# Optimization experiments

Measured on AMD Instinct MI355X. Metric: run time of the kernel, lower is better.

Reference implementation:

```python
import jax, jax.numpy as jnp
import numpy as np

B, S, E, H = 2, 2048, 1024, 16
D = E // H  # head_dim = 64


def setup_inputs() -> dict:
    key = jax.random.key(0)
    ks = jax.random.split(key, 5)
    return {
        "hidden_states": jax.random.normal(ks[0], (B, S, E), jnp.float32),
        "c_attn_w": jax.random.normal(ks[1], (E, 3 * E), jnp.float32) * 0.02,
        "c_attn_b": jnp.zeros((3 * E,), jnp.float32),
        "c_proj_w": jax.random.normal(ks[2], (E, E), jnp.float32) * 0.02,
        "c_proj_b": jnp.zeros((E,), jnp.float32),
    }


def reference(hidden_states, c_attn_w, c_attn_b, c_proj_w, c_proj_b):
    # Conv1D: x @ w + b -> qkv [B, S, 3E]
    qkv = hidden_states @ c_attn_w + c_attn_b
    q, k, v = jnp.split(qkv, 3, axis=-1)
    # [B, H, S, D]
    q = q.reshape(B, S, H, D).transpose(0, 2, 1, 3)
    k = k.reshape(B, S, H, D).transpose(0, 2, 1, 3)
    v = v.reshape(B, S, H, D).transpose(0, 2, 1, 3)
    # scores [B, H, S, S], scaled by sqrt(head_dim)
    scores = jnp.einsum("bhqd,bhkd->bhqk", q, k) / jnp.sqrt(jnp.asarray(D, q.dtype))
    causal = jnp.tril(jnp.ones((S, S), bool))  # [S, S]
    mask_value = jnp.finfo(scores.dtype).min
    scores = jnp.where(causal, scores, mask_value)
    attn = jax.nn.softmax(scores, axis=-1)
    # attn @ V -> [B, H, S, D] -> [B, S, E]
    out = jnp.einsum("bhqk,bhkd->bhqd", attn, v)
    out = out.transpose(0, 2, 1, 3).reshape(B, S, E)
    return out @ c_proj_w + c_proj_b
```

## Files before the change

### kernel.cpp

```cpp
#include <hip/hip_runtime.h>

using bf16 = __bf16;
typedef __bf16 bf16x8 __attribute__((ext_vector_type(8)));
typedef __bf16 bf16x4 __attribute__((ext_vector_type(4)));
typedef float  f32x4  __attribute__((ext_vector_type(4)));

#define MFMA16(a, b, c) __builtin_amdgcn_mfma_f32_16x16x32_bf16((a), (b), (c), 0, 0, 0)

static constexpr int S = 2048, E = 1024;
static constexpr float CSCALE = 0.18033688011112042f;

__device__ __forceinline__ void gld16(const bf16* g, bf16* l) {
    __builtin_amdgcn_global_load_lds((const __attribute__((address_space(1))) unsigned*)g,
                                     (__attribute__((address_space(3))) unsigned*)l, 16, 0, 0);
}

__global__ __launch_bounds__(256) void k_prep(const float* __restrict__ hs, const float* __restrict__ w0,
                                              const float* __restrict__ w1, bf16* __restrict__ A0,
                                              bf16* __restrict__ Wt0, bf16* __restrict__ Wt1) {
    __shared__ float tile[64][33];
    const int bx = blockIdx.x;
    if (bx < 4096) {
        int i = (bx * 256 + threadIdx.x) * 4;
        float4 v = *(const float4*)(hs + i);
        bf16x4 o = { (bf16)v.x, (bf16)v.y, (bf16)v.z, (bf16)v.w };
        *(bf16x4*)(A0 + i) = o;
        return;
    }
    const float* in;
    bf16* outp;
    int K, N, nb, kb;
    const int j = bx - 4096;
    if (j < 1536) { in = w0; outp = Wt0; K = 1024; N = 3072; nb = j % 96; kb = j / 96; }
    else          { in = w1; outp = Wt1; K = 1024; N = 1024; nb = (j - 1536) % 32; kb = (j - 1536) / 32; }
    const int bxx = nb * 32, byy = kb * 64;
    {
        const int r0 = threadIdx.x >> 5, c = threadIdx.x & 31;
#pragma unroll
        for (int i = 0; i < 8; i++)
            tile[r0 + i * 8][c] = in[(long)(byy + r0 + i * 8) * N + bxx + c];
    }
    __syncthreads();
    {
        const int n0 = threadIdx.x >> 6, k = threadIdx.x & 63;
#pragma unroll
        for (int i = 0; i < 8; i++) {
            const int n = n0 + i * 4;
            outp[(long)(bxx + n) * K + byy + k] = (bf16)tile[k][n];
        }
    }
}

__global__ __launch_bounds__(256) void k_gemm_qkv(const bf16* __restrict__ A, const bf16* __restrict__ Bt,
                                                  const float* __restrict__ bias, bf16* __restrict__ Qs,
                                                  bf16* __restrict__ Kf, bf16* __restrict__ Vf, int Kk) {
    const int bm = blockIdx.x * 128;
    const int bn = blockIdx.y * 128;
    const int tid = threadIdx.x;
    const int w = tid >> 6, lane = tid & 63;
    const int wm = (w >> 1) * 64, wn = (w & 1) * 64;
    const int col = lane & 15, quad = lane >> 4;

    __shared__ __align__(16) char smem[32768];
    bf16* sA = (bf16*)smem;
    bf16* sB = (bf16*)(smem + 16384);
    bf16* T  = (bf16*)smem;

    const bf16* pA[4]; const bf16* pB[4]; bf16* lA[4]; bf16* lB[4];
#pragma unroll
    for (int i = 0; i < 4; i++) {
        const int c = i * 256 + w * 64 + lane;
        const int r = c >> 3, sl = (c & 7) ^ (r & 7);
        pA[i] = A  + (long)(bm + r) * Kk + sl * 8;
        pB[i] = Bt + (long)(bn + r) * Kk + sl * 8;
        lA[i] = sA + i * 2048 + w * 512;
        lB[i] = sB + i * 2048 + w * 512;
    }

    f32x4 acc[4][4] = {};

    for (int k0 = 0; k0 < Kk; k0 += 64) {
        __syncthreads();
#pragma unroll
        for (int i = 0; i < 4; i++) gld16(pA[i] + k0, lA[i]);
#pragma unroll
        for (int i = 0; i < 4; i++) gld16(pB[i] + k0, lB[i]);
        __syncthreads();
#pragma unroll
        for (int h = 0; h < 2; h++) {
            bf16x8 af[4], bfr[4];
#pragma unroll
            for (int mt = 0; mt < 4; mt++) {
                const int row = wm + mt * 16 + col;
                af[mt] = *(const bf16x8*)(sA + row * 64 + (((h * 4 + quad) ^ (col & 7)) * 8));
            }
#pragma unroll
            for (int nt = 0; nt < 4; nt++) {
                const int row = wn + nt * 16 + col;
                bfr[nt] = *(const bf16x8*)(sB + row * 64 + (((h * 4 + quad) ^ (col & 7)) * 8));
            }
#pragma unroll
            for (int mt = 0; mt < 4; mt++)
#pragma unroll
                for (int nt = 0; nt < 4; nt++)
                    acc[mt][nt] = MFMA16(af[mt], bfr[nt], acc[mt][nt]);
        }
    }

    const int seg = bn >> 10;
    const int b = bm >> 11;
    const int kt0 = (bm & 2047) >> 6;

    if (seg == 0) {
#pragma unroll
        for (int mt = 0; mt < 4; mt++) {
            const int gr = bm + wm + mt * 16 + quad * 4;
#pragma unroll
            for (int nt = 0; nt < 4; nt++) {
                const int gc = bn + wn + nt * 16 + col;
                const float bv = bias[gc];
#pragma unroll
                for (int r = 0; r < 4; r++)
                    Qs[(long)(gr + r) * 1024 + gc] = (bf16)((acc[mt][nt][r] + bv) * CSCALE);
            }
        }
        return;
    }

    const int hl = w >> 1;
    if (seg == 1) {
        const int bh = b * 16 + (bn >> 6) - 16 + hl;
#pragma unroll 1
        for (int p = 0; p < 2; p++) {
            __syncthreads();
            if ((wm >> 6) == p) {
#pragma unroll
                for (int mt = 0; mt < 4; mt++) {
                    const int sl = mt * 16 + quad * 4;
#pragma unroll
                    for (int nt = 0; nt < 4; nt++) {
                        const int gcl = wn + nt * 16 + col;
                        const float bv = bias[bn + gcl];
#pragma unroll
                        for (int r = 0; r < 4; r++)
                            T[(sl + r) * 136 + gcl] = (bf16)(acc[mt][nt][r] + bv);
                    }
                }
            }
            __syncthreads();
            const int ktp = kt0 + p;
#pragma unroll
            for (int mi = 0; mi < 2; mi++) {
                const int mt = (w & 1) * 2 + mi;
#pragma unroll
                for (int half = 0; half < 2; half++) {
                    bf16x8 ch = *(const bf16x8*)(T + (mt * 16 + col) * 136 + hl * 64 + half * 32 + quad * 8);
                    const long chunk = ((long)(bh * 32 + ktp) * 8 + mt * 2 + half) * 64 + lane;
                    *(bf16x8*)(Kf + chunk * 8) = ch;
                }
            }
        }
    } else {
        const int bh = b * 16 + (bn >> 6) - 32 + hl;
#pragma unroll 1
        for (int p = 0; p < 2; p++) {
            __syncthreads();
            if ((wm >> 6) == p) {
#pragma unroll
                for (int mt = 0; mt < 4; mt++) {
                    const int sl = mt * 16 + quad * 4;
#pragma unroll
                    for (int nt = 0; nt < 4; nt++) {
                        const int gcl = wn + nt * 16 + col;
                        const float bv = bias[bn + gcl];
                        bf16x4 pk = { (bf16)(acc[mt][nt][0] + bv), (bf16)(acc[mt][nt][1] + bv),
                                      (bf16)(acc[mt][nt][2] + bv), (bf16)(acc[mt][nt][3] + bv) };
                        *(bf16x4*)(T + gcl * 72 + sl) = pk;
                    }
                }
            }
            __syncthreads();
            const int ktp = kt0 + p;
#pragma unroll
            for (int di = 0; di < 2; di++) {
                const int dt = (w & 1) * 2 + di;
#pragma unroll
                for (int ks = 0; ks < 2; ks++) {
                    bf16x8 ch = *(const bf16x8*)(T + (hl * 64 + dt * 16 + col) * 72 + ks * 32 + quad * 8);
                    const long chunk = ((long)(bh * 32 + ktp) * 8 + dt * 2 + ks) * 64 + lane;
                    *(bf16x8*)(Vf + chunk * 8) = ch;
                }
            }
        }
    }
}

__global__ __launch_bounds__(256) void k_gemm_bt64(const bf16* __restrict__ A, const bf16* __restrict__ Bt,
                                                    const float* __restrict__ bias, float* __restrict__ Cout,
                                                    int Mm, int Nn, int Kk) {
    const int bm = blockIdx.x * 64;
    const int bn = blockIdx.y * 128;
    const int tid = threadIdx.x;
    const int w = tid >> 6, lane = tid & 63;
    const int wm = (w >> 1) * 32, wn = (w & 1) * 64;
    const int col = lane & 15, quad = lane >> 4;

    __shared__ bf16 sA[64 * 64];
    __shared__ bf16 sB[128 * 64];

    const bf16* pA[2]; bf16* lA[2];
#pragma unroll
    for (int i = 0; i < 2; i++) {
        const int c = i * 256 + w * 64 + lane;
        const int r = c >> 3, sl = (c & 7) ^ (r & 7);
        pA[i] = A + (long)(bm + r) * Kk + sl * 8;
        lA[i] = sA + i * 2048 + w * 512;
    }
    const bf16* pB[4]; bf16* lB[4];
#pragma unroll
    for (int i = 0; i < 4; i++) {
        const int c = i * 256 + w * 64 + lane;
        const int r = c >> 3, sl = (c & 7) ^ (r & 7);
        pB[i] = Bt + (long)(bn + r) * Kk + sl * 8;
        lB[i] = sB + i * 2048 + w * 512;
    }

    f32x4 acc[2][4] = {};

    for (int k0 = 0; k0 < Kk; k0 += 64) {
        __syncthreads();
#pragma unroll
        for (int i = 0; i < 2; i++) gld16(pA[i] + k0, lA[i]);
#pragma unroll
        for (int i = 0; i < 4; i++) gld16(pB[i] + k0, lB[i]);
        __syncthreads();
#pragma unroll
        for (int h = 0; h < 2; h++) {
            bf16x8 af[2], bfr[4];
#pragma unroll
            for (int mt = 0; mt < 2; mt++) {
                const int row = wm + mt * 16 + col;
                af[mt] = *(const bf16x8*)(sA + row * 64 + (((h * 4 + quad) ^ (col & 7)) * 8));
            }
#pragma unroll
            for (int nt = 0; nt < 4; nt++) {
                const int row = wn + nt * 16 + col;
                bfr[nt] = *(const bf16x8*)(sB + row * 64 + (((h * 4 + quad) ^ (col & 7)) * 8));
            }
#pragma unroll
            for (int mt = 0; mt < 2; mt++)
#pragma unroll
                for (int nt = 0; nt < 4; nt++)
                    acc[mt][nt] = MFMA16(af[mt], bfr[nt], acc[mt][nt]);
        }
    }

#pragma unroll
    for (int mt = 0; mt < 2; mt++) {
        const int gr = bm + wm + mt * 16 + quad * 4;
#pragma unroll
        for (int nt = 0; nt < 4; nt++) {
            const int gc = bn + wn + nt * 16 + col;
            const float bv = bias[gc];
#pragma unroll
            for (int r = 0; r < 4; r++)
                Cout[(long)(gr + r) * Nn + gc] = acc[mt][nt][r] + bv;
        }
    }
}

__global__ __launch_bounds__(128, 2) void k_attn(const bf16* __restrict__ Qs, const bf16* __restrict__ Kf,
                                                 const bf16* __restrict__ Vf, bf16* __restrict__ out) {
    const int bh = blockIdx.x & 31;
    const int t = blockIdx.x >> 5;
    const int b = bh >> 4, h = bh & 15;
    const int tid = threadIdx.x;
    const int w = tid >> 6, lane = tid & 63;
    const int col = lane & 15, quad = lane >> 4;
    const int q0 = t * 64;
    const int nkt = t + 1;
    const int kA = nkt >> 1;
    const int kbeg = w ? kA : 0;
    const int kend = w ? nkt : kA;

    __shared__ bf16 sP[2][4096];
    __shared__ float M[64][73];
    bf16* pw = sP[w];

    const bf16* kfb = Kf + ((long)bh << 17) + lane * 8;
    const bf16* vfb = Vf + ((long)bh << 17) + lane * 8;

    bf16x8 bq[4][2];
#pragma unroll
    for (int qg = 0; qg < 4; qg++) {
        const bf16* qp = Qs + (long)(b * S + q0 + qg * 16 + col) * E + h * 64 + quad * 8;
        bq[qg][0] = *(const bf16x8*)(qp);
        bq[qg][1] = *(const bf16x8*)(qp + 32);
    }
    float m_[4] = { -1e30f, -1e30f, -1e30f, -1e30f }, l_[4] = { 0.f, 0.f, 0.f, 0.f };
    f32x4 o[4][4] = {};

#pragma unroll 1
    for (int kt = kbeg; kt < kend; kt++) {
        bf16x8 kfr[4][2], vfr[4][2];
#pragma unroll
        for (int mt = 0; mt < 4; mt++)
#pragma unroll
            for (int half = 0; half < 2; half++)
                kfr[mt][half] = *(const bf16x8*)(kfb + ((long)(kt * 8 + mt * 2 + half) << 9));
#pragma unroll
        for (int dt = 0; dt < 4; dt++)
#pragma unroll
            for (int ks = 0; ks < 2; ks++)
                vfr[dt][ks] = *(const bf16x8*)(vfb + ((long)(kt * 8 + dt * 2 + ks) << 9));

#pragma unroll
        for (int qg = 0; qg < 4; qg++) {
            f32x4 s[4];
#pragma unroll
            for (int mt = 0; mt < 4; mt++) {
                f32x4 z = {};
                z = MFMA16(kfr[mt][0], bq[qg][0], z);
                z = MFMA16(kfr[mt][1], bq[qg][1], z);
                s[mt] = z;
            }
            if (kt == nkt - 1) {
                const int qrow = q0 + qg * 16 + col;
#pragma unroll
                for (int mt = 0; mt < 4; mt++)
#pragma unroll
                    for (int r = 0; r < 4; r++)
                        if (kt * 64 + mt * 16 + quad * 4 + r > qrow) s[mt][r] = -1e30f;
            }
            float cm = -1e30f;
#pragma unroll
            for (int mt = 0; mt < 4; mt++)
#pragma unroll
                for (int r = 0; r < 4; r++) cm = fmaxf(cm, s[mt][r]);
            cm = fmaxf(cm, __shfl_xor(cm, 16));
            cm = fmaxf(cm, __shfl_xor(cm, 32));
            const float mnew = fmaxf(m_[qg], cm);
            const float alpha = __builtin_amdgcn_exp2f(m_[qg] - mnew);
            m_[qg] = mnew;
            float rs = 0.f;
#pragma unroll
            for (int mt = 0; mt < 4; mt++)
#pragma unroll
                for (int r = 0; r < 4; r++) {
                    float pe = __builtin_amdgcn_exp2f(s[mt][r] - mnew);
                    s[mt][r] = pe;
                    rs += pe;
                }
            l_[qg] = l_[qg] * alpha + rs;
#pragma unroll
            for (int dt = 0; dt < 4; dt++)
#pragma unroll
                for (int r = 0; r < 4; r++) o[qg][dt][r] *= alpha;
            const int q = qg * 16 + col;
#pragma unroll
            for (int mt = 0; mt < 4; mt++) {
                const int cl = mt * 2 + (quad >> 1);
                bf16x4 pk = { (bf16)s[mt][0], (bf16)s[mt][1], (bf16)s[mt][2], (bf16)s[mt][3] };
                *(bf16x4*)(pw + q * 64 + ((cl ^ (q & 7)) * 8 + (quad & 1) * 4)) = pk;
            }
        }
#pragma unroll
        for (int ks = 0; ks < 2; ks++) {
#pragma unroll
            for (int qg = 0; qg < 4; qg++) {
                const int q = qg * 16 + col;
                const bf16x8 ap = *(const bf16x8*)(pw + q * 64 + (((ks * 4 + quad) ^ (q & 7)) * 8));
#pragma unroll
                for (int dt = 0; dt < 4; dt++)
                    o[qg][dt] = MFMA16(vfr[dt][ks], ap, o[qg][dt]);
            }
        }
    }

#pragma unroll
    for (int qg = 0; qg < 4; qg++) {
        float lt = l_[qg];
        lt += __shfl_xor(lt, 16);
        lt += __shfl_xor(lt, 32);
        l_[qg] = lt;
    }

    if (w == 0) {
#pragma unroll
        for (int qg = 0; qg < 4; qg++) {
#pragma unroll
            for (int dt = 0; dt < 4; dt++)
#pragma unroll
                for (int r = 0; r < 4; r++)
                    M[lane][(qg * 4 + dt) * 4 + r] = o[qg][dt][r];
            M[lane][64 + qg * 2] = m_[qg];
            M[lane][65 + qg * 2] = l_[qg];
        }
    }
    __syncthreads();
    if (w == 1) {
#pragma unroll
        for (int qg = 0; qg < 4; qg++) {
            const float m0 = M[lane][64 + qg * 2];
            const float l0 = M[lane][65 + qg * 2];
            const float mm = fmaxf(m0, m_[qg]);
            const float a0 = __builtin_amdgcn_exp2f(m0 - mm);
            const float a1 = __builtin_amdgcn_exp2f(m_[qg] - mm);
            const float li = 1.f / (l0 * a0 + l_[qg] * a1);
            bf16* op = out + (long)(b * S + q0 + qg * 16 + col) * E + h * 64 + quad * 4;
#pragma unroll
            for (int dt = 0; dt < 4; dt++) {
                bf16x4 ov;
#pragma unroll
                for (int r = 0; r < 4; r++)
                    ov[r] = (bf16)((M[lane][(qg * 4 + dt) * 4 + r] * a0 + o[qg][dt][r] * a1) * li);
                *(bf16x4*)(op + dt * 16) = ov;
            }
        }
    }
}

extern "C" void kernel_launch(void* const* d_in, const int* in_sizes, int n_in,
                              void* d_out, int out_size, void* d_ws, size_t ws_size,
                              hipStream_t stream) {
    const float* hs = (const float*)d_in[0];
    const float* w0 = (const float*)d_in[1];
    const float* b0 = (const float*)d_in[2];
    const float* w1 = (const float*)d_in[3];
    const float* b1 = (const float*)d_in[4];
    float* outp = (float*)d_out;

    char* ws = (char*)d_ws;
    bf16* A0    = (bf16*)(ws);
    bf16* Wt0   = (bf16*)(ws + 8388608);
    bf16* Wt1   = (bf16*)(ws + 14680064);
    bf16* Qs    = (bf16*)(ws + 16777216);
    bf16* Kf    = (bf16*)(ws + 25165824);
    bf16* Vf    = (bf16*)(ws + 33554432);
    bf16* attnO = (bf16*)(ws + 41943040);

    k_prep<<<6144, 256, 0, stream>>>(hs, w0, w1, A0, Wt0, Wt1);
    k_gemm_qkv<<<dim3(32, 24), 256, 0, stream>>>(A0, Wt0, b0, Qs, Kf, Vf, 1024);
    k_attn<<<1024, 128, 0, stream>>>(Qs, Kf, Vf, attnO);
    k_gemm_bt64<<<dim3(64, 8), 256, 0, stream>>>(attnO, Wt1, b1, outp, 4096, 1024, 1024);
}
```

Before: 186.4 us.

## Pair causal query tiles per block and split KV across four waves

The attention kernel now has each block handle two query tiles, t and 31-t, one after the other, so every block does roughly the same causal work. The KV range of each tile is split across four waves instead of two, and the partial softmax states are merged through shared memory. This targets load imbalance from causal masking and is meant to expose more parallelism per tile. In exchange the block is larger, uses more shared memory, and adds extra barriers and a four-way merge for every tile.

New measurement: 193.7 us. 1.04x slower.

```diff
diff --git a/kernel.cpp b/kernel.cpp
--- a/kernel.cpp
+++ b/kernel.cpp
@@ -269,152 +269,164 @@
     }
 }
 
-__global__ __launch_bounds__(128, 2) void k_attn(const bf16* __restrict__ Qs, const bf16* __restrict__ Kf,
+__global__ __launch_bounds__(256, 2) void k_attn(const bf16* __restrict__ Qs, const bf16* __restrict__ Kf,
                                                  const bf16* __restrict__ Vf, bf16* __restrict__ out) {
     const int bh = blockIdx.x & 31;
-    const int t = blockIdx.x >> 5;
+    const int tp = blockIdx.x >> 5;
     const int b = bh >> 4, h = bh & 15;
     const int tid = threadIdx.x;
     const int w = tid >> 6, lane = tid & 63;
     const int col = lane & 15, quad = lane >> 4;
-    const int q0 = t * 64;
-    const int nkt = t + 1;
-    const int kA = nkt >> 1;
-    const int kbeg = w ? kA : 0;
-    const int kend = w ? nkt : kA;
-
-    __shared__ bf16 sP[2][4096];
-    __shared__ float M[64][73];
+
+    __shared__ bf16 sP[4][4096];
+    __shared__ float Mbuf[3 * 64 * 76];
     bf16* pw = sP[w];
 
     const bf16* kfb = Kf + ((long)bh << 17) + lane * 8;
     const bf16* vfb = Vf + ((long)bh << 17) + lane * 8;
 
-    bf16x8 bq[4][2];
-#pragma unroll
-    for (int qg = 0; qg < 4; qg++) {
-        const bf16* qp = Qs + (long)(b * S + q0 + qg * 16 + col) * E + h * 64 + quad * 8;
-        bq[qg][0] = *(const bf16x8*)(qp);
-        bq[qg][1] = *(const bf16x8*)(qp + 32);
-    }
-    float m_[4] = { -1e30f, -1e30f, -1e30f, -1e30f }, l_[4] = { 0.f, 0.f, 0.f, 0.f };
-    f32x4 o[4][4] = {};
-
 #pragma unroll 1
-    for (int kt = kbeg; kt < kend; kt++) {
-        bf16x8 kfr[4][2], vfr[4][2];
-#pragma unroll
-        for (int mt = 0; mt < 4; mt++)
-#pragma unroll
-            for (int half = 0; half < 2; half++)
-                kfr[mt][half] = *(const bf16x8*)(kfb + ((long)(kt * 8 + mt * 2 + half) << 9));
-#pragma unroll
-        for (int dt = 0; dt < 4; dt++)
-#pragma unroll
-            for (int ks = 0; ks < 2; ks++)
-                vfr[dt][ks] = *(const bf16x8*)(vfb + ((long)(kt * 8 + dt * 2 + ks) << 9));
-
+    for (int sel = 0; sel < 2; sel++) {
+        const int t = sel ? 31 - tp : tp;
+        const int q0 = t * 64;
+        const int nkt = t + 1;
+        const int kbeg = (nkt * w) >> 2;
+        const int kend = (nkt * (w + 1)) >> 2;
+
+        bf16x8 bq[4][2];
 #pragma unroll
         for (int qg = 0; qg < 4; qg++) {
-            f32x4 s[4];
-#pragma unroll
-            for (int mt = 0; mt < 4; mt++) {
-                f32x4 z = {};
-                z = MFMA16(kfr[mt][0], bq[qg][0], z);
-                z = MFMA16(kfr[mt][1], bq[qg][1], z);
-                s[mt] = z;
-            }
-            if (kt == nkt - 1) {
-                const int qrow = q0 + qg * 16 + col;
+            const bf16* qp = Qs + (long)(b * S + q0 + qg * 16 + col) * E + h * 64 + quad * 8;
+            bq[qg][0] = *(const bf16x8*)(qp);
+            bq[qg][1] = *(const bf16x8*)(qp + 32);
+        }
+        float m_[4] = { -1e30f, -1e30f, -1e30f, -1e30f }, l_[4] = { 0.f, 0.f, 0.f, 0.f };
+        f32x4 o[4][4] = {};
+
+#pragma unroll 1
+        for (int kt = kbeg; kt < kend; kt++) {
+            bf16x8 kfr[4][2], vfr[4][2];
+#pragma unroll
+            for (int mt = 0; mt < 4; mt++)
+#pragma unroll
+                for (int half = 0; half < 2; half++)
+                    kfr[mt][half] = *(const bf16x8*)(kfb + ((long)(kt * 8 + mt * 2 + half) << 9));
+#pragma unroll
+            for (int dt = 0; dt < 4; dt++)
+#pragma unroll
+                for (int ks = 0; ks < 2; ks++)
+                    vfr[dt][ks] = *(const bf16x8*)(vfb + ((long)(kt * 8 + dt * 2 + ks) << 9));
+
+#pragma unroll
+            for (int qg = 0; qg < 4; qg++) {
+                f32x4 s[4];
+#pragma unroll
+                for (int mt = 0; mt < 4; mt++) {
+                    f32x4 z = {};
+                    z = MFMA16(kfr[mt][0], bq[qg][0], z);
+                    z = MFMA16(kfr[mt][1], bq[qg][1], z);
+                    s[mt] = z;
+                }
+                if (kt == nkt - 1) {
+                    const int qrow = q0 + qg * 16 + col;
+#pragma unroll
+                    for (int mt = 0; mt < 4; mt++)
+#pragma unroll
+                        for (int r = 0; r < 4; r++)
+                            if (kt * 64 + mt * 16 + quad * 4 + r > qrow) s[mt][r] = -1e30f;
+                }
+                float cm = -1e30f;
 #pragma unroll
                 for (int mt = 0; mt < 4; mt++)
 #pragma unroll
-                    for (int r = 0; r < 4; r++)
-                        if (kt * 64 + mt * 16 + quad * 4 + r > qrow) s[mt][r] = -1e30f;
-            }
-            float cm = -1e30f;
-#pragma unroll
-            for (int mt = 0; mt < 4; mt++)
-#pragma unroll
-                for (int r = 0; r < 4; r++) cm = fmaxf(cm, s[mt][r]);
-            cm = fmaxf(cm, __shfl_xor(cm, 16));
-            cm = fmaxf(cm, __shfl_xor(cm, 32));
-            const float mnew = fmaxf(m_[qg], cm);
-            const float alpha = __builtin_amdgcn_exp2f(m_[qg] - mnew);
-            m_[qg] = mnew;
-            float rs = 0.f;
-#pragma unroll
-            for (int mt = 0; mt < 4; mt++)
-#pragma unroll
-                for (int r = 0; r < 4; r++) {
-                    float pe = __builtin_amdgcn_exp2f(s[mt][r] - mnew);
-                    s[mt][r] = pe;
-                    rs += pe;
-                }
-            l_[qg] = l_[qg] * alpha + rs;
-#pragma unroll
-            for (int dt = 0; dt < 4; dt++)
-#pragma unroll
-                for (int r = 0; r < 4; r++) o[qg][dt][r] *= alpha;
-            const int q = qg * 16 + col;
-#pragma unroll
-            for (int mt = 0; mt < 4; mt++) {
-                const int cl = mt * 2 + (quad >> 1);
-                bf16x4 pk = { (bf16)s[mt][0], (bf16)s[mt][1], (bf16)s[mt][2], (bf16)s[mt][3] };
-                *(bf16x4*)(pw + q * 64 + ((cl ^ (q & 7)) * 8 + (quad & 1) * 4)) = pk;
-            }
-        }
-#pragma unroll
-        for (int ks = 0; ks < 2; ks++) {
+                    for (int r = 0; r < 4; r++) cm = fmaxf(cm, s[mt][r]);
+                cm = fmaxf(cm, __shfl_xor(cm, 16));
+                cm = fmaxf(cm, __shfl_xor(cm, 32));
+                const float mnew = fmaxf(m_[qg], cm);
+                const float alpha = __builtin_amdgcn_exp2f(m_[qg] - mnew);
+                m_[qg] = mnew;
+                float rs = 0.f;
+#pragma unroll
+                for (int mt = 0; mt < 4; mt++)
+#pragma unroll
+                    for (int r = 0; r < 4; r++) {
+                        float pe = __builtin_amdgcn_exp2f(s[mt][r] - mnew);
+                        s[mt][r] = pe;
+                        rs += pe;
+                    }
+                l_[qg] = l_[qg] * alpha + rs;
+#pragma unroll
+                for (int dt = 0; dt < 4; dt++)
+#pragma unroll
+                    for (int r = 0; r < 4; r++) o[qg][dt][r] *= alpha;
+                const int q = qg * 16 + col;
+#pragma unroll
+                for (int mt = 0; mt < 4; mt++) {
+                    const int cl = mt * 2 + (quad >> 1);
+                    bf16x4 pk = { (bf16)s[mt][0], (bf16)s[mt][1], (bf16)s[mt][2], (bf16)s[mt][3] };
+                    *(bf16x4*)(pw + q * 64 + ((cl ^ (q & 7)) * 8 + (quad & 1) * 4)) = pk;
+                }
+            }
+#pragma unroll
+            for (int ks = 0; ks < 2; ks++) {
+#pragma unroll
+                for (int qg = 0; qg < 4; qg++) {
+                    const int q = qg * 16 + col;
+                    const bf16x8 ap = *(const bf16x8*)(pw + q * 64 + (((ks * 4 + quad) ^ (q & 7)) * 8));
+#pragma unroll
+                    for (int dt = 0; dt < 4; dt++)
+                        o[qg][dt] = MFMA16(vfr[dt][ks], ap, o[qg][dt]);
+                }
+            }
+        }
+
+#pragma unroll
+        for (int qg = 0; qg < 4; qg++) {
+            float lt = l_[qg];
+            lt += __shfl_xor(lt, 16);
+            lt += __shfl_xor(lt, 32);
+            l_[qg] = lt;
+        }
+
+        __syncthreads();
+        if (w > 0) {
+            float* mp = Mbuf + ((w - 1) * 64 + lane) * 76;
 #pragma unroll
             for (int qg = 0; qg < 4; qg++) {
-                const int q = qg * 16 + col;
-                const bf16x8 ap = *(const bf16x8*)(pw + q * 64 + (((ks * 4 + quad) ^ (q & 7)) * 8));
 #pragma unroll
                 for (int dt = 0; dt < 4; dt++)
-                    o[qg][dt] = MFMA16(vfr[dt][ks], ap, o[qg][dt]);
-            }
-        }
-    }
-
-#pragma unroll
-    for (int qg = 0; qg < 4; qg++) {
-        float lt = l_[qg];
-        lt += __shfl_xor(lt, 16);
-        lt += __shfl_xor(lt, 32);
-        l_[qg] = lt;
-    }
-
-    if (w == 0) {
-#pragma unroll
-        for (int qg = 0; qg < 4; qg++) {
-#pragma unroll
-            for (int dt = 0; dt < 4; dt++)
-#pragma unroll
-                for (int r = 0; r < 4; r++)
-                    M[lane][(qg * 4 + dt) * 4 + r] = o[qg][dt][r];
-            M[lane][64 + qg * 2] = m_[qg];
-            M[lane][65 + qg * 2] = l_[qg];
-        }
-    }
-    __syncthreads();
-    if (w == 1) {
-#pragma unroll
-        for (int qg = 0; qg < 4; qg++) {
-            const float m0 = M[lane][64 + qg * 2];
-            const float l0 = M[lane][65 + qg * 2];
-            const float mm = fmaxf(m0, m_[qg]);
-            const float a0 = __builtin_amdgcn_exp2f(m0 - mm);
-            const float a1 = __builtin_amdgcn_exp2f(m_[qg] - mm);
-            const float li = 1.f / (l0 * a0 + l_[qg] * a1);
-            bf16* op = out + (long)(b * S + q0 + qg * 16 + col) * E + h * 64 + quad * 4;
-#pragma unroll
-            for (int dt = 0; dt < 4; dt++) {
-                bf16x4 ov;
-#pragma unroll
-                for (int r = 0; r < 4; r++)
-                    ov[r] = (bf16)((M[lane][(qg * 4 + dt) * 4 + r] * a0 + o[qg][dt][r] * a1) * li);
-                *(bf16x4*)(op + dt * 16) = ov;
+                    *(f32x4*)(mp + (qg * 4 + dt) * 4) = o[qg][dt];
+                mp[64 + qg * 2] = m_[qg];
+                mp[65 + qg * 2] = l_[qg];
+            }
+        }
+        __syncthreads();
+        if (w == 0) {
+            const float* mp0 = Mbuf + lane * 76;
+            const float* mp1 = Mbuf + (64 + lane) * 76;
+            const float* mp2 = Mbuf + (128 + lane) * 76;
+#pragma unroll
+            for (int qg = 0; qg < 4; qg++) {
+                const float m1 = mp0[64 + qg * 2], l1 = mp0[65 + qg * 2];
+                const float m2 = mp1[64 + qg * 2], l2 = mp1[65 + qg * 2];
+                const float m3 = mp2[64 + qg * 2], l3 = mp2[65 + qg * 2];
+                const float mm = fmaxf(fmaxf(m_[qg], m1), fmaxf(m2, m3));
+                const float a0 = __builtin_amdgcn_exp2f(m_[qg] - mm);
+                const float a1 = __builtin_amdgcn_exp2f(m1 - mm);
+                const float a2 = __builtin_amdgcn_exp2f(m2 - mm);
+                const float a3 = __builtin_amdgcn_exp2f(m3 - mm);
+                const float li = 1.f / (l_[qg] * a0 + l1 * a1 + l2 * a2 + l3 * a3);
+                bf16* op = out + (long)(b * S + q0 + qg * 16 + col) * E + h * 64 + quad * 4;
+#pragma unroll
+                for (int dt = 0; dt < 4; dt++) {
+                    f32x4 acc = o[qg][dt] * a0;
+                    acc += (*(const f32x4*)(mp0 + (qg * 4 + dt) * 4)) * a1;
+                    acc += (*(const f32x4*)(mp1 + (qg * 4 + dt) * 4)) * a2;
+                    acc += (*(const f32x4*)(mp2 + (qg * 4 + dt) * 4)) * a3;
+                    bf16x4 ov = { (bf16)(acc[0] * li), (bf16)(acc[1] * li),
+                                  (bf16)(acc[2] * li), (bf16)(acc[3] * li) };
+                    *(bf16x4*)(op + dt * 16) = ov;
+                }
             }
         }
     }
@@ -441,6 +453,6 @@
 
     k_prep<<<6144, 256, 0, stream>>>(hs, w0, w1, A0, Wt0, Wt1);
     k_gemm_qkv<<<dim3(32, 24), 256, 0, stream>>>(A0, Wt0, b0, Qs, Kf, Vf, 1024);
-    k_attn<<<1024, 128, 0, stream>>>(Qs, Kf, Vf, attnO);
+    k_attn<<<512, 256, 0, stream>>>(Qs, Kf, Vf, attnO);
     k_gemm_bt64<<<dim3(64, 8), 256, 0, stream>>>(attnO, Wt1, b1, outp, 4096, 1024, 1024);
 }
```
